# Kernel optimization log

Measured on AMD Instinct MI355X. Metric: run time of the kernel, lower is better.

The kernel has to match this reference:

```python
import jax, jax.numpy as jnp
import numpy as np

N, F_IN, F, H = 4096, 64, 64, 8


def setup_inputs() -> dict:
    key = jax.random.key(0)
    k1, k2, k3 = jax.random.split(key, 3)
    graph = jax.random.normal(k1, (N, F_IN), dtype=jnp.float32)
    # per-head Dense weights (no bias): W maps F_IN -> F, a maps 2F -> 1
    W = jax.random.normal(k2, (H, F_IN, F), dtype=jnp.float32) / np.sqrt(F_IN)
    a = jax.random.normal(k3, (H, 2 * F), dtype=jnp.float32) / np.sqrt(2 * F)
    return {"graph": graph, "W": W, "a": a}


def reference(graph, W, a):
    # ltg[h] = graph @ W[h]  -> [H, N, F]
    ltg = jnp.einsum('nf,hfk->hnk', graph, W)
    Fdim = W.shape[-1]
    a_src, a_dst = a[:, :Fdim], a[:, Fdim:]  # concat attention decomposes additively
    s = jnp.einsum('hnk,hk->hn', ltg, a_src)  # contribution of node i (row)
    d = jnp.einsum('hnk,hk->hn', ltg, a_dst)  # contribution of node j (col)
    # E[h,i,j] = leaky_relu(a_src.ltg[i] + a_dst.ltg[j])  -> [H, N, N]
    E = jax.nn.leaky_relu(s[:, :, None] + d[:, None, :], negative_slope=0.2)
    Alpha = jax.nn.softmax(E, axis=-1)
    # H_out[h] = Alpha[h] @ ltg[h]  -> [H, N, F]
    return jnp.einsum('hij,hjk->hik', Alpha, ltg)
```

## Files before the change

### kernel.cpp

```cpp
#include <hip/hip_runtime.h>
#include <hip/hip_bf16.h>

typedef __bf16 bf16x8 __attribute__((ext_vector_type(8)));
typedef float f32x4 __attribute__((ext_vector_type(4)));

static constexpr int NN = 4096;
static constexpr int FE = 64;
static constexpr int NH = 8;
#define LOG2E 1.44269504088896340736f

#if __has_builtin(__builtin_amdgcn_exp2f)
#define EXP2F(x) __builtin_amdgcn_exp2f(x)
#else
#define EXP2F(x) exp2f(x)
#endif

__global__ __launch_bounds__(256) void gat_k1(
    const float* __restrict__ graph, const float* __restrict__ W,
    const float* __restrict__ a, ushort* __restrict__ ltgT,
    float* __restrict__ st, float* __restrict__ dt)
{
  const int h  = blockIdx.y;
  const int n0 = blockIdx.x * 64;
  const int t  = threadIdx.x;

  __shared__ float  Wl[64 * 68];
  __shared__ float  gT[64 * 68];
  __shared__ ushort lt[64 * 64];

  const float* Wh = W + h * FE * FE;
  const int fr = t >> 2;
  const int qc = (t & 3) * 16;
  #pragma unroll
  for (int e = 0; e < 4; e++) {
    float4 wv = *(const float4*)(Wh + fr * FE + qc + e * 4);
    *(float4*)(&Wl[fr * 68 + qc + e * 4]) = wv;
    float4 gv = *(const float4*)(graph + (n0 + fr) * FE + qc + e * 4);
    gT[(qc + e * 4 + 0) * 68 + fr] = gv.x;
    gT[(qc + e * 4 + 1) * 68 + fr] = gv.y;
    gT[(qc + e * 4 + 2) * 68 + fr] = gv.z;
    gT[(qc + e * 4 + 3) * 68 + fr] = gv.w;
  }
  __syncthreads();

  const int n4 = (t >> 4) * 4;
  const int k4 = (t & 15) * 4;
  float acc[4][4];
  #pragma unroll
  for (int i = 0; i < 4; i++)
    #pragma unroll
    for (int j = 0; j < 4; j++) acc[i][j] = 0.f;

  for (int f = 0; f < FE; f++) {
    f32x4 g = *(const f32x4*)(&gT[f * 68 + n4]);
    f32x4 w = *(const f32x4*)(&Wl[f * 68 + k4]);
    #pragma unroll
    for (int i = 0; i < 4; i++)
      #pragma unroll
      for (int j = 0; j < 4; j++)
        acc[i][j] = fmaf(g[i], w[j], acc[i][j]);
  }

  float4 As = *(const float4*)(a + h * 2 * FE + k4);
  float4 Ad = *(const float4*)(a + h * 2 * FE + FE + k4);
  float sp[4], dp[4];
  #pragma unroll
  for (int i = 0; i < 4; i++) {
    sp[i] = acc[i][0] * As.x + acc[i][1] * As.y + acc[i][2] * As.z + acc[i][3] * As.w;
    dp[i] = acc[i][0] * Ad.x + acc[i][1] * Ad.y + acc[i][2] * Ad.z + acc[i][3] * Ad.w;
  }
  #pragma unroll
  for (int off = 1; off < 16; off <<= 1) {
    #pragma unroll
    for (int i = 0; i < 4; i++) {
      sp[i] += __shfl_xor(sp[i], off);
      dp[i] += __shfl_xor(dp[i], off);
    }
  }
  if ((t & 15) == 0) {
    #pragma unroll
    for (int i = 0; i < 4; i++) {
      st[h * NN + n0 + n4 + i] = sp[i] * LOG2E;
      dt[h * NN + n0 + n4 + i] = dp[i] * LOG2E;
    }
  }

  #pragma unroll
  for (int i = 0; i < 4; i++)
    #pragma unroll
    for (int j = 0; j < 4; j++) {
      __bf16 b = (__bf16)acc[i][j];
      lt[(k4 + j) * 64 + (n4 + i)] = __builtin_bit_cast(unsigned short, b);
    }
  __syncthreads();

  const int kk = t >> 2;
  const int nc = (t & 3) * 16;
  uint4 v0 = *(const uint4*)(&lt[kk * 64 + nc]);
  uint4 v1 = *(const uint4*)(&lt[kk * 64 + nc + 8]);
  ushort* dst = ltgT + (size_t)h * FE * NN + kk * NN + n0 + nc;
  *(uint4*)(dst) = v0;
  *(uint4*)(dst + 8) = v1;
}

__global__ __launch_bounds__(256, 2) void gat_k2(
    const ushort* __restrict__ ltgT, const float* __restrict__ st,
    const float* __restrict__ dt, float* __restrict__ out)
{
  const int h    = blockIdx.y;
  const int i0   = blockIdx.x * 64;
  const int w    = threadIdx.x >> 6;
  const int lane = threadIdx.x & 63;
  const int col  = lane & 15;
  const int koff = (lane >> 4) * 8;

  __shared__ float lds_pacc[4][64 * 68];
  __shared__ float lds_z[4][64];

  const float*  dh  = dt + h * NN;
  const ushort* lth = ltgT + (size_t)h * FE * NN;

  float sr[4];
  #pragma unroll
  for (int g = 0; g < 4; g++) sr[g] = st[h * NN + i0 + g * 16 + col];

  f32x4 acc[4][4], accZ[4];
  #pragma unroll
  for (int g = 0; g < 4; g++) {
    #pragma unroll
    for (int tt = 0; tt < 4; tt++) acc[g][tt] = (f32x4){0.f, 0.f, 0.f, 0.f};
    accZ[g] = (f32x4){0.f, 0.f, 0.f, 0.f};
  }

  bf16x8 ones;
  #pragma unroll
  for (int e = 0; e < 8; e++) ones[e] = (__bf16)1.0f;

  const int jbeg = w * (NN / 4);
  for (int j0 = jbeg; j0 < jbeg + NN / 4; j0 += 64) {
    const float* dp = dh + j0 + koff;
    float4 dA = *(const float4*)(dp);
    float4 dB = *(const float4*)(dp + 4);
    float4 dC = *(const float4*)(dp + 32);
    float4 dD = *(const float4*)(dp + 36);
    float dv[16] = {dA.x, dA.y, dA.z, dA.w, dB.x, dB.y, dB.z, dB.w,
                    dC.x, dC.y, dC.z, dC.w, dD.x, dD.y, dD.z, dD.w};

    bf16x8 bfr[4][2];
    #pragma unroll
    for (int tt = 0; tt < 4; tt++)
      #pragma unroll
      for (int ks = 0; ks < 2; ks++)
        bfr[tt][ks] = *(const bf16x8*)(const void*)(lth + (size_t)(tt * 16 + col) * NN + j0 + ks * 32 + koff);

    #pragma unroll
    for (int g = 0; g < 4; g++) {
      bf16x8 af[2];
      #pragma unroll
      for (int ks = 0; ks < 2; ks++) {
        #pragma unroll
        for (int e = 0; e < 8; e++) {
          const float x = sr[g] + dv[ks * 8 + e];
          af[ks][e] = (__bf16)EXP2F(fmaxf(x, 0.2f * x));
        }
      }
      #pragma unroll
      for (int tt = 0; tt < 4; tt++) {
        #pragma unroll
        for (int ks = 0; ks < 2; ks++)
          acc[g][tt] = __builtin_amdgcn_mfma_f32_16x16x32_bf16(af[ks], bfr[tt][ks], acc[g][tt], 0, 0, 0);
      }
      #pragma unroll
      for (int ks = 0; ks < 2; ks++)
        accZ[g] = __builtin_amdgcn_mfma_f32_16x16x32_bf16(af[ks], ones, accZ[g], 0, 0, 0);
    }
  }

  const int rquad = (lane >> 4) * 4;
  #pragma unroll
  for (int g = 0; g < 4; g++) {
    if (col == 0) {
      #pragma unroll
      for (int reg = 0; reg < 4; reg++) lds_z[w][g * 16 + rquad + reg] = accZ[g][reg];
    }
    #pragma unroll
    for (int tt = 0; tt < 4; tt++) {
      #pragma unroll
      for (int reg = 0; reg < 4; reg++)
        lds_pacc[w][(g * 16 + rquad + reg) * 68 + tt * 16 + col] = acc[g][tt][reg];
    }
  }
  __syncthreads();

  const int r   = threadIdx.x >> 2;
  const int f16 = (threadIdx.x & 3) * 16;
  f32x4 s0 = (f32x4){0.f,0.f,0.f,0.f}, s1 = s0, s2 = s0, s3 = s0;
  float zz = 0.f;
  #pragma unroll
  for (int ww = 0; ww < 4; ww++) {
    const float* pp = &lds_pacc[ww][r * 68 + f16];
    s0 += *(const f32x4*)(pp);
    s1 += *(const f32x4*)(pp + 4);
    s2 += *(const f32x4*)(pp + 8);
    s3 += *(const f32x4*)(pp + 12);
    zz += lds_z[ww][r];
  }
  const float inv = 1.f / zz;
  float* orow = &out[((size_t)h * NN + i0 + r) * FE + f16];
  f32x4 o0 = {s0[0]*inv, s0[1]*inv, s0[2]*inv, s0[3]*inv};
  f32x4 o1 = {s1[0]*inv, s1[1]*inv, s1[2]*inv, s1[3]*inv};
  f32x4 o2 = {s2[0]*inv, s2[1]*inv, s2[2]*inv, s2[3]*inv};
  f32x4 o3 = {s3[0]*inv, s3[1]*inv, s3[2]*inv, s3[3]*inv};
  *(f32x4*)(orow)      = o0;
  *(f32x4*)(orow + 4)  = o1;
  *(f32x4*)(orow + 8)  = o2;
  *(f32x4*)(orow + 12) = o3;
}

extern "C" void kernel_launch(void* const* d_in, const int* in_sizes, int n_in,
                              void* d_out, int out_size, void* d_ws, size_t ws_size,
                              hipStream_t stream) {
  const float* graph = (const float*)d_in[0];
  const float* W     = (const float*)d_in[1];
  const float* a     = (const float*)d_in[2];
  float* outp        = (float*)d_out;

  char* p = (char*)d_ws;
  ushort* ltgT = (ushort*)p;              p += (size_t)NH * FE * NN * 2;
  float*  st   = (float*)p;               p += (size_t)NH * NN * 4;
  float*  dtp  = (float*)p;               p += (size_t)NH * NN * 4;

  dim3 g1(NN / 64, NH);
  gat_k1<<<g1, 256, 0, stream>>>(graph, W, a, ltgT, st, dtp);
  dim3 g2(NN / 64, NH);
  gat_k2<<<g2, 256, 0, stream>>>(ltgT, st, dtp, outp);
}
```

Baseline: 106.3 us.

## Use bf16 MFMA for projection and precompute W·a for attention scores

```diff
diff --git a/kernel.cpp b/kernel.cpp
--- a/kernel.cpp
+++ b/kernel.cpp
@@ -15,89 +15,111 @@
 #define EXP2F(x) exp2f(x)
 #endif
 
+static __device__ __forceinline__ ushort bf16_bits(float x) {
+  __bf16 b = (__bf16)x;
+  return __builtin_bit_cast(unsigned short, b);
+}
+
 __global__ __launch_bounds__(256) void gat_k1(
     const float* __restrict__ graph, const float* __restrict__ W,
     const float* __restrict__ a, ushort* __restrict__ ltgT,
     float* __restrict__ st, float* __restrict__ dt)
 {
-  const int h  = blockIdx.y;
-  const int n0 = blockIdx.x * 64;
-  const int t  = threadIdx.x;
-
-  __shared__ float  Wl[64 * 68];
-  __shared__ float  gT[64 * 68];
-  __shared__ ushort lt[64 * 64];
+  const int h    = blockIdx.y;
+  const int n0   = blockIdx.x * 64;
+  const int t    = threadIdx.x;
+  const int w    = t >> 6;
+  const int lane = t & 63;
+  const int col  = lane & 15;
+  const int koff = (lane >> 4) * 8;
+
+  __shared__ ushort WtL[64 * 72];
+  __shared__ ushort lt[64 * 72];
+  __shared__ float  waL[2][64];
 
   const float* Wh = W + h * FE * FE;
-  const int fr = t >> 2;
-  const int qc = (t & 3) * 16;
-  #pragma unroll
-  for (int e = 0; e < 4; e++) {
-    float4 wv = *(const float4*)(Wh + fr * FE + qc + e * 4);
-    *(float4*)(&Wl[fr * 68 + qc + e * 4]) = wv;
-    float4 gv = *(const float4*)(graph + (n0 + fr) * FE + qc + e * 4);
-    gT[(qc + e * 4 + 0) * 68 + fr] = gv.x;
-    gT[(qc + e * 4 + 1) * 68 + fr] = gv.y;
-    gT[(qc + e * 4 + 2) * 68 + fr] = gv.z;
-    gT[(qc + e * 4 + 3) * 68 + fr] = gv.w;
+
+  {
+    const int f  = t >> 2;
+    const int kc = (t & 3) * 16;
+    #pragma unroll
+    for (int e = 0; e < 4; e++) {
+      float4 wv = *(const float4*)(Wh + f * FE + kc + e * 4);
+      WtL[(kc + e * 4 + 0) * 72 + f] = bf16_bits(wv.x);
+      WtL[(kc + e * 4 + 1) * 72 + f] = bf16_bits(wv.y);
+      WtL[(kc + e * 4 + 2) * 72 + f] = bf16_bits(wv.z);
+      WtL[(kc + e * 4 + 3) * 72 + f] = bf16_bits(wv.w);
+    }
+  }
+
+  if (t < 128) {
+    const int sd = t >> 6;
+    const int f  = t & 63;
+    const float* av = a + h * 2 * FE + sd * FE;
+    const float* wr = Wh + f * FE;
+    float s = 0.f;
+    #pragma unroll
+    for (int k = 0; k < FE; k += 4) {
+      float4 wv = *(const float4*)(wr + k);
+      float4 av4 = *(const float4*)(av + k);
+      s += wv.x * av4.x + wv.y * av4.y + wv.z * av4.z + wv.w * av4.w;
+    }
+    waL[sd][f] = s;
   }
   __syncthreads();
 
-  const int n4 = (t >> 4) * 4;
-  const int k4 = (t & 15) * 4;
-  float acc[4][4];
-  #pragma unroll
-  for (int i = 0; i < 4; i++)
-    #pragma unroll
-    for (int j = 0; j < 4; j++) acc[i][j] = 0.f;
-
-  for (int f = 0; f < FE; f++) {
-    f32x4 g = *(const f32x4*)(&gT[f * 68 + n4]);
-    f32x4 w = *(const f32x4*)(&Wl[f * 68 + k4]);
-    #pragma unroll
-    for (int i = 0; i < 4; i++)
-      #pragma unroll
-      for (int j = 0; j < 4; j++)
-        acc[i][j] = fmaf(g[i], w[j], acc[i][j]);
-  }
-
-  float4 As = *(const float4*)(a + h * 2 * FE + k4);
-  float4 Ad = *(const float4*)(a + h * 2 * FE + FE + k4);
-  float sp[4], dp[4];
-  #pragma unroll
-  for (int i = 0; i < 4; i++) {
-    sp[i] = acc[i][0] * As.x + acc[i][1] * As.y + acc[i][2] * As.z + acc[i][3] * As.w;
-    dp[i] = acc[i][0] * Ad.x + acc[i][1] * Ad.y + acc[i][2] * Ad.z + acc[i][3] * Ad.w;
-  }
-  #pragma unroll
-  for (int off = 1; off < 16; off <<= 1) {
-    #pragma unroll
-    for (int i = 0; i < 4; i++) {
-      sp[i] += __shfl_xor(sp[i], off);
-      dp[i] += __shfl_xor(dp[i], off);
-    }
-  }
-  if ((t & 15) == 0) {
-    #pragma unroll
-    for (int i = 0; i < 4; i++) {
-      st[h * NN + n0 + n4 + i] = sp[i] * LOG2E;
-      dt[h * NN + n0 + n4 + i] = dp[i] * LOG2E;
-    }
-  }
-
-  #pragma unroll
-  for (int i = 0; i < 4; i++)
-    #pragma unroll
-    for (int j = 0; j < 4; j++) {
-      __bf16 b = (__bf16)acc[i][j];
-      lt[(k4 + j) * 64 + (n4 + i)] = __builtin_bit_cast(unsigned short, b);
-    }
+  f32x4 acc[4];
+  #pragma unroll
+  for (int tt = 0; tt < 4; tt++) acc[tt] = (f32x4){0.f, 0.f, 0.f, 0.f};
+
+  bf16x8 afr[2];
+  const float* grow = graph + (size_t)(n0 + w * 16 + col) * FE;
+  #pragma unroll
+  for (int ks = 0; ks < 2; ks++) {
+    float4 a0 = *(const float4*)(grow + ks * 32 + koff);
+    float4 a1 = *(const float4*)(grow + ks * 32 + koff + 4);
+    afr[ks][0] = (__bf16)a0.x; afr[ks][1] = (__bf16)a0.y;
+    afr[ks][2] = (__bf16)a0.z; afr[ks][3] = (__bf16)a0.w;
+    afr[ks][4] = (__bf16)a1.x; afr[ks][5] = (__bf16)a1.y;
+    afr[ks][6] = (__bf16)a1.z; afr[ks][7] = (__bf16)a1.w;
+  }
+  #pragma unroll
+  for (int tt = 0; tt < 4; tt++) {
+    #pragma unroll
+    for (int ks = 0; ks < 2; ks++) {
+      bf16x8 bf = *(const bf16x8*)(const void*)(&WtL[(tt * 16 + col) * 72 + ks * 32 + koff]);
+      acc[tt] = __builtin_amdgcn_mfma_f32_16x16x32_bf16(afr[ks], bf, acc[tt], 0, 0, 0);
+    }
+  }
+
+  if (t < 128) {
+    const int sd = t >> 6;
+    const int n  = t & 63;
+    const float* gr = graph + (size_t)(n0 + n) * FE;
+    float s = 0.f;
+    #pragma unroll
+    for (int k = 0; k < FE; k += 4) {
+      float4 g4 = *(const float4*)(gr + k);
+      s += g4.x * waL[sd][k] + g4.y * waL[sd][k + 1] +
+           g4.z * waL[sd][k + 2] + g4.w * waL[sd][k + 3];
+    }
+    float* outp = sd ? dt : st;
+    outp[h * NN + n0 + n] = s * LOG2E;
+  }
+
+  const int rquad = (lane >> 4) * 4;
+  #pragma unroll
+  for (int tt = 0; tt < 4; tt++) {
+    #pragma unroll
+    for (int reg = 0; reg < 4; reg++)
+      lt[(tt * 16 + col) * 72 + w * 16 + rquad + reg] = bf16_bits(acc[tt][reg]);
+  }
   __syncthreads();
 
   const int kk = t >> 2;
   const int nc = (t & 3) * 16;
-  uint4 v0 = *(const uint4*)(&lt[kk * 64 + nc]);
-  uint4 v1 = *(const uint4*)(&lt[kk * 64 + nc + 8]);
+  uint4 v0 = *(const uint4*)(&lt[kk * 72 + nc]);
+  uint4 v1 = *(const uint4*)(&lt[kk * 72 + nc + 8]);
   ushort* dst = ltgT + (size_t)h * FE * NN + kk * NN + n0 + nc;
   *(uint4*)(dst) = v0;
   *(uint4*)(dst + 8) = v1;
```

New measurement: 106.0 us. No clear change (-0.3%).
